# Kernel tuning notes

Measured on AMD Instinct MI355X. Metric: run time of the kernel, lower is better.

Reference implementation:

```python
import jax, jax.numpy as jnp
import numpy as np

D = 256
H1, H2 = 256, 128

def setup_inputs() -> dict:
    key0 = jax.random.key(0)
    ks = jax.random.split(key0, 10)
    B, Lq, Lk = 2, 512, 512
    query = jax.random.normal(ks[0], (B, Lq, D), dtype=jnp.float32)
    key_t = jax.random.normal(ks[1], (B, Lk, D), dtype=jnp.float32)
    value = jax.random.normal(ks[2], (B, Lk, D), dtype=jnp.float32)
    mask = jnp.ones((B, Lq, Lk), dtype=jnp.int32)
    s1 = 1.0 / np.sqrt(2 * D)
    W1 = jax.random.uniform(ks[3], (2 * D, H1), jnp.float32, -s1, s1)  # torch Linear(2D,H1), [in,out]
    b1 = jax.random.uniform(ks[4], (H1,), jnp.float32, -s1, s1)
    s2 = 1.0 / np.sqrt(H1)
    W2 = jax.random.uniform(ks[5], (H1, H2), jnp.float32, -s2, s2)
    b2 = jax.random.uniform(ks[6], (H2,), jnp.float32, -s2, s2)
    s3 = 1.0 / np.sqrt(H2)
    W3 = jax.random.uniform(ks[7], (H2, 1), jnp.float32, -s3, s3)
    b3 = jax.random.uniform(ks[8], (1,), jnp.float32, -s3, s3)
    return {"query": query, "key": key_t, "value": value, "mask": mask,
            "W1": W1, "b1": b1, "W2": W2, "b2": b2, "W3": W3, "b3": b3}

def reference(query, key, value, mask, W1, b1, W2, b2, W3, b3):
    # Original: cat([q_i, k_j]) @ W1 == q_i @ W1[:D] + k_j @ W1[D:]  (algebraic split,
    # identical math, avoids materializing the [B,Lq,Lk,2D] concat tensor).
    W1q, W1k = W1[:D], W1[D:]
    qp = jnp.einsum('bqd,dh->bqh', query, W1q)           # [B,Lq,H1]
    kp = jnp.einsum('bkd,dh->bkh', key, W1k)             # [B,Lk,H1]
    h1 = jax.nn.relu(qp[:, :, None, :] + kp[:, None, :, :] + b1)   # [B,Lq,Lk,H1]
    h2 = jax.nn.relu(jnp.einsum('bqkh,hj->bqkj', h1, W2) + b2)      # [B,Lq,Lk,H2]
    scores = (jnp.einsum('bqkj,jo->bqko', h2, W3) + b3)[..., 0]     # [B,Lq,Lk]
    scores = jnp.where(mask == 0, jnp.float32(-1e9), scores)
    attn = jax.nn.softmax(scores, axis=-1)               # dropout is identity in eval mode
    out = jnp.einsum('bqk,bkd->bqd', attn, value)
    return out, attn
```

## Files before the change

kernel.cpp:

```cpp
#include <hip/hip_runtime.h>

#define D_  256
#define H1_ 256
#define H2_ 128
#define B_  2
#define LQ_ 512
#define LK_ 512
#define BK  64

typedef float  f32x4  __attribute__((ext_vector_type(4)));
typedef __bf16 bf16x8 __attribute__((ext_vector_type(8)));
typedef __bf16 bf16x4 __attribute__((ext_vector_type(4)));

__global__ __launch_bounds__(512) void prep_kernel(
    const float* __restrict__ query, const float* __restrict__ key,
    const float* __restrict__ W1, const float* __restrict__ b1,
    const float* __restrict__ W2,
    float* __restrict__ qp, float* __restrict__ kp, __bf16* __restrict__ w2t) {
  const int blk = blockIdx.x;
  const int tid = threadIdx.x;
  if (blk >= 512) {
    const int id = (blk - 512) * 512 + tid;
    const int n = id >> 8;
    const int k = id & 255;
    w2t[n * H1_ + k] = (__bf16)W2[k * H2_ + n];
    return;
  }
  __shared__ float in_lds[4][D_];
  __shared__ float part[4][H1_];
  const int row0 = blk * 4;
  const int sel  = row0 >> 10;
  const float* __restrict__ src = sel ? key : query;
  const int base = (row0 & 1023) * D_;
  for (int i = tid; i < 4 * D_; i += 512)
    in_lds[i >> 8][i & 255] = src[base + i];
  __syncthreads();
  const int h  = tid & 255;
  const int kh = tid >> 8;
  float acc[4] = {0.f, 0.f, 0.f, 0.f};
  const float* __restrict__ w = W1 + sel * D_ * H1_ + kh * 128 * H1_ + h;
#pragma unroll 4
  for (int dd = 0; dd < 128; ++dd) {
    const float wv = w[dd * H1_];
    const int d = kh * 128 + dd;
#pragma unroll
    for (int r = 0; r < 4; ++r) acc[r] += in_lds[r][d] * wv;
  }
  if (kh == 1) {
#pragma unroll
    for (int r = 0; r < 4; ++r) part[r][h] = acc[r];
  }
  __syncthreads();
  if (kh == 0) {
    const float bias = sel ? 0.0f : b1[h];
    float* __restrict__ dst = sel ? kp : qp;
#pragma unroll
    for (int r = 0; r < 4; ++r)
      dst[base + r * H1_ + h] = acc[r] + part[r][h] + bias;
  }
}

__global__ __launch_bounds__(256, 2) void score_kernel(
    const float* __restrict__ qp, const float* __restrict__ kp,
    const __bf16* __restrict__ w2t,
    const float* __restrict__ b2, const float* __restrict__ W3,
    const float* __restrict__ b3, float* __restrict__ scores) {
  __shared__ __align__(16) __bf16 A_lds[128 * BK];
  __shared__ __align__(16) __bf16 B_lds[128 * BK];
  __shared__ float  spart[2][128];

  const int b  = blockIdx.z;
  const int q0 = blockIdx.y * 8;
  const int k0 = blockIdx.x * 16;
  const int tid  = threadIdx.x;
  const int wave = tid >> 6;
  const int lane = tid & 63;
  const int quad = lane >> 4;
  const int l16  = lane & 15;
  const int wm   = wave >> 1;
  const int wn   = wave & 1;
  const int h8   = l16 & 7;

  const float* __restrict__ qpb = qp + (b * LQ_ + q0) * H1_;
  const float* __restrict__ kpb = kp + (b * LK_ + k0) * H1_;

  f32x4 acc[4][4];
#pragma unroll
  for (int mt = 0; mt < 4; ++mt)
#pragma unroll
    for (int nt = 0; nt < 4; ++nt)
      acc[mt][nt] = (f32x4){0.f, 0.f, 0.f, 0.f};

  for (int kc = 0; kc < H1_ / BK; ++kc) {
#pragma unroll
    for (int i = 0; i < 8; ++i) {
      const int r  = i * 16 + (tid >> 4);
      const int kg = tid & 15;
      const int qi = r >> 4, ki = r & 15;
      const int kcol = kc * BK + kg * 4;
      const float4 qv = *(const float4*)(qpb + qi * H1_ + kcol);
      const float4 kv = *(const float4*)(kpb + ki * H1_ + kcol);
      bf16x4 a;
      a[0] = (__bf16)fmaxf(qv.x + kv.x, 0.f);
      a[1] = (__bf16)fmaxf(qv.y + kv.y, 0.f);
      a[2] = (__bf16)fmaxf(qv.z + kv.z, 0.f);
      a[3] = (__bf16)fmaxf(qv.w + kv.w, 0.f);
      const int sw = (((kg >> 1) ^ (r & 7)) << 3) + ((kg & 1) << 2);
      *(bf16x4*)(&A_lds[r * BK + sw]) = a;
    }
#pragma unroll
    for (int i = 0; i < 4; ++i) {
      const int u = i * 256 + tid;
      const int n = u >> 3, c = u & 7;
      *(uint4*)(&B_lds[n * BK + ((c ^ (n & 7)) << 3)]) =
          *(const uint4*)(w2t + n * H1_ + kc * BK + c * 8);
    }
    __syncthreads();
#pragma unroll
    for (int ks = 0; ks < BK / 32; ++ks) {
      const int cbase = ks * 4 + quad;
      bf16x8 af[4], bfr[4];
#pragma unroll
      for (int mt = 0; mt < 4; ++mt) {
        const int ra = wm * 64 + mt * 16 + l16;
        af[mt] = *(const bf16x8*)(&A_lds[ra * BK + ((cbase ^ h8) << 3)]);
      }
#pragma unroll
      for (int nt = 0; nt < 4; ++nt) {
        const int rb = wn * 64 + nt * 16 + l16;
        bfr[nt] = *(const bf16x8*)(&B_lds[rb * BK + ((cbase ^ h8) << 3)]);
      }
#pragma unroll
      for (int mt = 0; mt < 4; ++mt)
#pragma unroll
        for (int nt = 0; nt < 4; ++nt)
          acc[mt][nt] = __builtin_amdgcn_mfma_f32_16x16x32_bf16(
              af[mt], bfr[nt], acc[mt][nt], 0, 0, 0);
    }
    __syncthreads();
  }

  float part[4][4];
#pragma unroll
  for (int mt = 0; mt < 4; ++mt)
#pragma unroll
    for (int rg = 0; rg < 4; ++rg) part[mt][rg] = 0.f;
#pragma unroll
  for (int nt = 0; nt < 4; ++nt) {
    const int col = wn * 64 + nt * 16 + l16;
    const float b2v = b2[col];
    const float w3v = W3[col];
#pragma unroll
    for (int mt = 0; mt < 4; ++mt)
#pragma unroll
      for (int rg = 0; rg < 4; ++rg) {
        float h2 = acc[mt][nt][rg] + b2v;
        h2 = fmaxf(h2, 0.f);
        part[mt][rg] += h2 * w3v;
      }
  }
#pragma unroll
  for (int off = 1; off < 16; off <<= 1)
#pragma unroll
    for (int mt = 0; mt < 4; ++mt)
#pragma unroll
      for (int rg = 0; rg < 4; ++rg)
        part[mt][rg] += __shfl_xor(part[mt][rg], off, 64);
  if (l16 == 0) {
#pragma unroll
    for (int mt = 0; mt < 4; ++mt)
#pragma unroll
      for (int rg = 0; rg < 4; ++rg) {
        const int rl = wm * 64 + mt * 16 + quad * 4 + rg;
        spart[wn][rl] = part[mt][rg];
      }
  }
  __syncthreads();
  if (tid < 128) {
    const float s = spart[0][tid] + spart[1][tid] + b3[0];
    const int qi = tid >> 4, ki = tid & 15;
    scores[(b * LQ_ + q0 + qi) * LK_ + k0 + ki] = s;
  }
}

__global__ void softmax_kernel(float* __restrict__ attn,
                               const int* __restrict__ mask) {
  const int row = blockIdx.x;
  const int tid = threadIdx.x;
  __shared__ float redm[4];
  __shared__ float reds[4];
  float* __restrict__ arow = attn + row * LK_;
  const int* __restrict__ mrow = mask + row * LK_;
  float s0 = arow[tid], s1 = arow[tid + 256];
  if (mrow[tid] == 0)       s0 = -1e9f;
  if (mrow[tid + 256] == 0) s1 = -1e9f;
  float m = fmaxf(s0, s1);
#pragma unroll
  for (int off = 32; off; off >>= 1) m = fmaxf(m, __shfl_xor(m, off, 64));
  if ((tid & 63) == 0) redm[tid >> 6] = m;
  __syncthreads();
  m = fmaxf(fmaxf(redm[0], redm[1]), fmaxf(redm[2], redm[3]));
  const float e0 = __expf(s0 - m), e1 = __expf(s1 - m);
  float sum = e0 + e1;
#pragma unroll
  for (int off = 32; off; off >>= 1) sum += __shfl_xor(sum, off, 64);
  if ((tid & 63) == 0) reds[tid >> 6] = sum;
  __syncthreads();
  sum = reds[0] + reds[1] + reds[2] + reds[3];
  const float inv = 1.f / sum;
  arow[tid]       = e0 * inv;
  arow[tid + 256] = e1 * inv;
}

__global__ __launch_bounds__(512) void out_kernel2(
    const float* __restrict__ attn, const float* __restrict__ value,
    float* __restrict__ out) {
  const int ds = blockIdx.x, qg = blockIdx.y, b = blockIdx.z;
  const int tid = threadIdx.x;
  __shared__ float a_lds[8][LK_];
  __shared__ float p_lds[3][8][128];
  const float* __restrict__ abase = attn + (b * LQ_ + qg * 8) * LK_;
  for (int i = tid; i < 8 * LK_; i += 512)
    a_lds[i >> 9][i & 511] = abase[i];
  __syncthreads();
  const int dl = tid & 127;
  const int d  = dl + ds * 128;
  const int kh = tid >> 7;
  float acc[8] = {0.f, 0.f, 0.f, 0.f, 0.f, 0.f, 0.f, 0.f};
  const float* __restrict__ vb = value + (b * LK_ + kh * 128) * D_ + d;
#pragma unroll 4
  for (int k = 0; k < 128; ++k) {
    const float v = vb[k * D_];
    const float* __restrict__ ar = &a_lds[0][kh * 128 + k];
#pragma unroll
    for (int q = 0; q < 8; ++q) acc[q] += ar[q * LK_] * v;
  }
  if (kh > 0) {
#pragma unroll
    for (int q = 0; q < 8; ++q) p_lds[kh - 1][q][dl] = acc[q];
  }
  __syncthreads();
  if (kh == 0) {
    float* __restrict__ ob = out + (b * LQ_ + qg * 8) * D_ + d;
#pragma unroll
    for (int q = 0; q < 8; ++q)
      ob[q * D_] = acc[q] + p_lds[0][q][dl] + p_lds[1][q][dl] + p_lds[2][q][dl];
  }
}

extern "C" void kernel_launch(void* const* d_in, const int* in_sizes, int n_in,
                              void* d_out, int out_size, void* d_ws, size_t ws_size,
                              hipStream_t stream) {
  (void)in_sizes; (void)n_in; (void)out_size; (void)ws_size;
  const float* query = (const float*)d_in[0];
  const float* key   = (const float*)d_in[1];
  const float* value = (const float*)d_in[2];
  const int*   mask  = (const int*)d_in[3];
  const float* W1    = (const float*)d_in[4];
  const float* b1    = (const float*)d_in[5];
  const float* W2    = (const float*)d_in[6];
  const float* b2    = (const float*)d_in[7];
  const float* W3    = (const float*)d_in[8];
  const float* b3    = (const float*)d_in[9];

  float* out  = (float*)d_out;
  float* attn = out + B_ * LQ_ * D_;

  float*  qp  = (float*)d_ws;
  float*  kp  = qp + B_ * LQ_ * H1_;
  __bf16* w2t = (__bf16*)(kp + B_ * LK_ * H1_);

  prep_kernel<<<576, 512, 0, stream>>>(query, key, W1, b1, W2, qp, kp, w2t);
  dim3 gscore(LK_ / 16, LQ_ / 8, B_);
  score_kernel<<<gscore, 256, 0, stream>>>(qp, kp, w2t, b2, W3, b3, attn);
  softmax_kernel<<<B_ * LQ_, 256, 0, stream>>>(attn, mask);
  out_kernel2<<<dim3(2, 64, B_), 512, 0, stream>>>(attn, value, out);
}
```

Measured before the change: 152.6 us.

## Preswizzle W2 into MFMA fragments, load B from global, fuse softmax into output GEMM

The prep kernel now writes W2 in per-lane MFMA fragment order, so the score kernel loads B operands straight from global into registers and no longer stages them in LDS, halving LDS use. The A-tile build is reorganised so each thread loads its qp vector once and reuses it across eight key rows. Softmax is fused into the attn·V kernel: each block computes softmax for its 8 rows in registers, keeps the probabilities in LDS and writes attn once. This removes one launch and one round trip of the score matrix, at the cost of duplicating the softmax in both d-split blocks and adding register pressure in the score kernel.

```diff
diff --git a/kernel.cpp b/kernel.cpp
--- a/kernel.cpp
+++ b/kernel.cpp
@@ -16,14 +16,21 @@
     const float* __restrict__ query, const float* __restrict__ key,
     const float* __restrict__ W1, const float* __restrict__ b1,
     const float* __restrict__ W2,
-    float* __restrict__ qp, float* __restrict__ kp, __bf16* __restrict__ w2t) {
+    float* __restrict__ qp, float* __restrict__ kp, __bf16* __restrict__ w2f) {
   const int blk = blockIdx.x;
   const int tid = threadIdx.x;
   if (blk >= 512) {
-    const int id = (blk - 512) * 512 + tid;
-    const int n = id >> 8;
-    const int k = id & 255;
-    w2t[n * H1_ + k] = (__bf16)W2[k * H2_ + n];
+    const int id   = (blk - 512) * 512 + tid;
+    const int j    = id & 7;
+    const int lane = (id >> 3) & 63;
+    const int frag = id >> 9;
+    const int nt = frag & 3;
+    const int wn = (frag >> 2) & 1;
+    const int ks = (frag >> 3) & 1;
+    const int kc = frag >> 4;
+    const int n = wn * 64 + nt * 16 + (lane & 15);
+    const int k = kc * 64 + ks * 32 + ((lane >> 4) << 3) + j;
+    w2f[id] = (__bf16)W2[k * H2_ + n];
     return;
   }
   __shared__ float in_lds[4][D_];
@@ -62,11 +69,10 @@
 
 __global__ __launch_bounds__(256, 2) void score_kernel(
     const float* __restrict__ qp, const float* __restrict__ kp,
-    const __bf16* __restrict__ w2t,
+    const __bf16* __restrict__ w2f,
     const float* __restrict__ b2, const float* __restrict__ W3,
     const float* __restrict__ b3, float* __restrict__ scores) {
   __shared__ __align__(16) __bf16 A_lds[128 * BK];
-  __shared__ __align__(16) __bf16 B_lds[128 * BK];
   __shared__ float  spart[2][128];
 
   const int b  = blockIdx.z;
@@ -81,6 +87,10 @@
   const int wn   = wave & 1;
   const int h8   = l16 & 7;
 
+  const int qi = tid >> 5;
+  const int t5 = (tid >> 4) & 1;
+  const int kg = tid & 15;
+
   const float* __restrict__ qpb = qp + (b * LQ_ + q0) * H1_;
   const float* __restrict__ kpb = kp + (b * LK_ + k0) * H1_;
 
@@ -92,14 +102,20 @@
       acc[mt][nt] = (f32x4){0.f, 0.f, 0.f, 0.f};
 
   for (int kc = 0; kc < H1_ / BK; ++kc) {
-#pragma unroll
-    for (int i = 0; i < 8; ++i) {
-      const int r  = i * 16 + (tid >> 4);
-      const int kg = tid & 15;
-      const int qi = r >> 4, ki = r & 15;
-      const int kcol = kc * BK + kg * 4;
-      const float4 qv = *(const float4*)(qpb + qi * H1_ + kcol);
-      const float4 kv = *(const float4*)(kpb + ki * H1_ + kcol);
+    bf16x8 bfr[2][4];
+#pragma unroll
+    for (int ks = 0; ks < 2; ++ks)
+#pragma unroll
+      for (int nt = 0; nt < 4; ++nt)
+        bfr[ks][nt] = *(const bf16x8*)(
+            w2f + ((((kc * 2 + ks) * 2 + wn) * 4 + nt) * 64 + lane) * 8);
+
+    const float4 qv = *(const float4*)(qpb + qi * H1_ + kc * BK + kg * 4);
+#pragma unroll
+    for (int ii = 0; ii < 8; ++ii) {
+      const int ki = t5 * 8 + ii;
+      const int r  = qi * 16 + ki;
+      const float4 kv = *(const float4*)(kpb + ki * H1_ + kc * BK + kg * 4);
       bf16x4 a;
       a[0] = (__bf16)fmaxf(qv.x + kv.x, 0.f);
       a[1] = (__bf16)fmaxf(qv.y + kv.y, 0.f);
@@ -108,34 +124,22 @@
       const int sw = (((kg >> 1) ^ (r & 7)) << 3) + ((kg & 1) << 2);
       *(bf16x4*)(&A_lds[r * BK + sw]) = a;
     }
-#pragma unroll
-    for (int i = 0; i < 4; ++i) {
-      const int u = i * 256 + tid;
-      const int n = u >> 3, c = u & 7;
-      *(uint4*)(&B_lds[n * BK + ((c ^ (n & 7)) << 3)]) =
-          *(const uint4*)(w2t + n * H1_ + kc * BK + c * 8);
-    }
     __syncthreads();
 #pragma unroll
-    for (int ks = 0; ks < BK / 32; ++ks) {
+    for (int ks = 0; ks < 2; ++ks) {
       const int cbase = ks * 4 + quad;
-      bf16x8 af[4], bfr[4];
+      bf16x8 af[4];
 #pragma unroll
       for (int mt = 0; mt < 4; ++mt) {
         const int ra = wm * 64 + mt * 16 + l16;
         af[mt] = *(const bf16x8*)(&A_lds[ra * BK + ((cbase ^ h8) << 3)]);
       }
 #pragma unroll
-      for (int nt = 0; nt < 4; ++nt) {
-        const int rb = wn * 64 + nt * 16 + l16;
-        bfr[nt] = *(const bf16x8*)(&B_lds[rb * BK + ((cbase ^ h8) << 3)]);
-      }
-#pragma unroll
       for (int mt = 0; mt < 4; ++mt)
 #pragma unroll
         for (int nt = 0; nt < 4; ++nt)
           acc[mt][nt] = __builtin_amdgcn_mfma_f32_16x16x32_bf16(
-              af[mt], bfr[nt], acc[mt][nt], 0, 0, 0);
+              af[mt], bfr[ks][nt], acc[mt][nt], 0, 0, 0);
     }
     __syncthreads();
   }
@@ -178,50 +182,50 @@
   __syncthreads();
   if (tid < 128) {
     const float s = spart[0][tid] + spart[1][tid] + b3[0];
-    const int qi = tid >> 4, ki = tid & 15;
-    scores[(b * LQ_ + q0 + qi) * LK_ + k0 + ki] = s;
-  }
-}
-
-__global__ void softmax_kernel(float* __restrict__ attn,
-                               const int* __restrict__ mask) {
-  const int row = blockIdx.x;
-  const int tid = threadIdx.x;
-  __shared__ float redm[4];
-  __shared__ float reds[4];
-  float* __restrict__ arow = attn + row * LK_;
-  const int* __restrict__ mrow = mask + row * LK_;
-  float s0 = arow[tid], s1 = arow[tid + 256];
-  if (mrow[tid] == 0)       s0 = -1e9f;
-  if (mrow[tid + 256] == 0) s1 = -1e9f;
-  float m = fmaxf(s0, s1);
-#pragma unroll
-  for (int off = 32; off; off >>= 1) m = fmaxf(m, __shfl_xor(m, off, 64));
-  if ((tid & 63) == 0) redm[tid >> 6] = m;
-  __syncthreads();
-  m = fmaxf(fmaxf(redm[0], redm[1]), fmaxf(redm[2], redm[3]));
-  const float e0 = __expf(s0 - m), e1 = __expf(s1 - m);
-  float sum = e0 + e1;
-#pragma unroll
-  for (int off = 32; off; off >>= 1) sum += __shfl_xor(sum, off, 64);
-  if ((tid & 63) == 0) reds[tid >> 6] = sum;
-  __syncthreads();
-  sum = reds[0] + reds[1] + reds[2] + reds[3];
-  const float inv = 1.f / sum;
-  arow[tid]       = e0 * inv;
-  arow[tid + 256] = e1 * inv;
-}
-
-__global__ __launch_bounds__(512) void out_kernel2(
-    const float* __restrict__ attn, const float* __restrict__ value,
+    const int qi2 = tid >> 4, ki2 = tid & 15;
+    scores[(b * LQ_ + q0 + qi2) * LK_ + k0 + ki2] = s;
+  }
+}
+
+__global__ __launch_bounds__(512) void smout_kernel(
+    const float* __restrict__ sc, float* __restrict__ attn,
+    const int* __restrict__ mask, const float* __restrict__ value,
     float* __restrict__ out) {
   const int ds = blockIdx.x, qg = blockIdx.y, b = blockIdx.z;
   const int tid = threadIdx.x;
   __shared__ float a_lds[8][LK_];
   __shared__ float p_lds[3][8][128];
-  const float* __restrict__ abase = attn + (b * LQ_ + qg * 8) * LK_;
-  for (int i = tid; i < 8 * LK_; i += 512)
-    a_lds[i >> 9][i & 511] = abase[i];
+  const int row0 = b * LQ_ + qg * 8;
+  const int w = tid >> 6, lane = tid & 63;
+  {
+    const float* __restrict__ srow = sc + (row0 + w) * LK_;
+    const int*  __restrict__ mrow = mask + (row0 + w) * LK_;
+    float v[8];
+#pragma unroll
+    for (int j = 0; j < 8; ++j) {
+      float s = srow[lane + j * 64];
+      if (mrow[lane + j * 64] == 0) s = -1e9f;
+      v[j] = s;
+    }
+    float m = v[0];
+#pragma unroll
+    for (int j = 1; j < 8; ++j) m = fmaxf(m, v[j]);
+#pragma unroll
+    for (int off = 32; off; off >>= 1) m = fmaxf(m, __shfl_xor(m, off, 64));
+    float sum = 0.f;
+#pragma unroll
+    for (int j = 0; j < 8; ++j) { v[j] = __expf(v[j] - m); sum += v[j]; }
+#pragma unroll
+    for (int off = 32; off; off >>= 1) sum += __shfl_xor(sum, off, 64);
+    const float inv = 1.f / sum;
+    float* __restrict__ arow = attn + (row0 + w) * LK_;
+#pragma unroll
+    for (int j = 0; j < 8; ++j) {
+      const float p = v[j] * inv;
+      a_lds[w][lane + j * 64] = p;
+      if (ds == 0) arow[lane + j * 64] = p;
+    }
+  }
   __syncthreads();
   const int dl = tid & 127;
   const int d  = dl + ds * 128;
@@ -241,7 +245,7 @@
   }
   __syncthreads();
   if (kh == 0) {
-    float* __restrict__ ob = out + (b * LQ_ + qg * 8) * D_ + d;
+    float* __restrict__ ob = out + row0 * D_ + d;
 #pragma unroll
     for (int q = 0; q < 8; ++q)
       ob[q * D_] = acc[q] + p_lds[0][q][dl] + p_lds[1][q][dl] + p_lds[2][q][dl];
@@ -268,11 +272,11 @@
 
   float*  qp  = (float*)d_ws;
   float*  kp  = qp + B_ * LQ_ * H1_;
-  __bf16* w2t = (__bf16*)(kp + B_ * LK_ * H1_);
-
-  prep_kernel<<<576, 512, 0, stream>>>(query, key, W1, b1, W2, qp, kp, w2t);
+  __bf16* w2f = (__bf16*)(kp + B_ * LK_ * H1_);
+  float*  sc  = (float*)(w2f + H2_ * H1_);
+
+  prep_kernel<<<576, 512, 0, stream>>>(query, key, W1, b1, W2, qp, kp, w2f);
   dim3 gscore(LK_ / 16, LQ_ / 8, B_);
-  score_kernel<<<gscore, 256, 0, stream>>>(qp, kp, w2t, b2, W3, b3, attn);
-  softmax_kernel<<<B_ * LQ_, 256, 0, stream>>>(attn, mask);
-  out_kernel2<<<dim3(2, 64, B_), 512, 0, stream>>>(attn, value, out);
-}
+  score_kernel<<<gscore, 256, 0, stream>>>(qp, kp, w2f, b2, W3, b3, sc);
+  smout_kernel<<<dim3(2, 64, B_), 512, 0, stream>>>(sc, attn, mask, value, out);
+}
```

Measured after the change: 147.7 us. 1.03x faster.
